# Kernel optimization log

Hardware: AMD Instinct MI355X
Metric: run time of the kernel (lower is better)

Reference implementation:

```python
import jax, jax.numpy as jnp
import numpy as np
import math

D_MODEL = 1024
N_HEADS = 16
SEQ = 1024
BATCH = 4


def setup_inputs() -> dict:
    key = jax.random.key(0)
    ks = jax.random.split(key, 13)
    s = 1.0 / math.sqrt(D_MODEL)  # keep logits in a sane range
    return {
        "x": jax.random.normal(ks[0], (BATCH, SEQ, D_MODEL), jnp.float32),
        "Wq": jax.random.normal(ks[1], (D_MODEL, D_MODEL), jnp.float32) * s,
        "bq": jnp.zeros((D_MODEL,), jnp.float32),
        "Wk": jax.random.normal(ks[2], (D_MODEL, D_MODEL), jnp.float32) * s,
        "bk": jnp.zeros((D_MODEL,), jnp.float32),
        "Wv": jax.random.normal(ks[3], (D_MODEL, D_MODEL), jnp.float32) * s,
        "bv": jnp.zeros((D_MODEL,), jnp.float32),
        "Wo": jax.random.normal(ks[4], (D_MODEL, D_MODEL), jnp.float32) * s,
        "bo": jnp.zeros((D_MODEL,), jnp.float32),
        "Wimp": jax.random.normal(ks[5], (N_HEADS, D_MODEL), jnp.float32) * s,
        "bimp": jnp.zeros((N_HEADS,), jnp.float32),
        "k_ema": jax.random.normal(ks[6], (SEQ, D_MODEL), jnp.float32),
        "v_ema": jax.random.normal(ks[7], (SEQ, D_MODEL), jnp.float32),
    }


def reference(x, Wq, bq, Wk, bk, Wv, bv, Wo, bo, Wimp, bimp, k_ema, v_ema):
    B, S, D = x.shape
    H = Wimp.shape[0]
    hd = D // H

    def proj(W, b):
        # [B,S,D] -> [B,H,S,hd]
        return (x @ W.T + b).reshape(B, S, H, hd).transpose(0, 2, 1, 3)

    q = proj(Wq, bq)
    k = proj(Wk, bk)
    v = proj(Wv, bv)

    scores = jnp.einsum("bhqd,bhkd->bhqk", q, k) / math.sqrt(hd)

    # importance bias: outer-sum of per-head key/value importance vectors
    k_imp = (k_ema[:S] @ Wimp.T + bimp).T  # [H, S]
    v_imp = (v_ema[:S] @ Wimp.T + bimp).T  # [H, S]
    bias = 0.5 * (k_imp[:, :, None] + v_imp[:, None, :])  # [H, S, S]
    scores = scores + 0.1 * bias[None]

    # causal mask (torch masks before bias add; -inf + finite == -inf, so equivalent)
    causal = jnp.triu(jnp.ones((S, S), bool), k=1)
    scores = jnp.where(causal, -jnp.inf, scores)

    attn = jax.nn.softmax(scores, axis=-1)
    out = jnp.einsum("bhqk,bhkd->bhqd", attn, v)
    out = out.transpose(0, 2, 1, 3).reshape(B, S, D)
    return out @ Wo.T + bo
```

## Files before the change

kernel.cpp:

```cpp
#include <hip/hip_runtime.h>
#include <hip/hip_bf16.h>
#include <math.h>

#define D_MODEL 1024
#define SEQ     1024
#define BATCH   4
#define NHEADS  16
#define HD      64

#define QSC 0.18033688f
#define BSC 0.072134752f

typedef __bf16 bf16x8 __attribute__((ext_vector_type(8)));
typedef __bf16 bf16x4 __attribute__((ext_vector_type(4)));
typedef float  f32x4  __attribute__((ext_vector_type(4)));

__device__ __forceinline__ f32x4 mfma16(bf16x8 a, bf16x8 b, f32x4 c) {
  return __builtin_amdgcn_mfma_f32_16x16x32_bf16(a, b, c, 0, 0, 0);
}

__device__ __forceinline__ void async16(__bf16* lds, const __bf16* g) {
  __builtin_amdgcn_global_load_lds(g, lds, 16, 0, 0);
}

__device__ __forceinline__ float fexp2(float x) {
  float r;
  asm volatile("v_exp_f32 %0, %1" : "=v"(r) : "v"(x));
  return r;
}

__global__ __launch_bounds__(256) void prep_kernel(
    const float* __restrict__ x,
    const float* __restrict__ Wq, const float* __restrict__ Wk,
    const float* __restrict__ Wv, const float* __restrict__ Wo,
    const float* __restrict__ v_ema,
    const float* __restrict__ Wimp, const float* __restrict__ bimp,
    __bf16* __restrict__ x_bf, __bf16* __restrict__ wq_bf, __bf16* __restrict__ wk_bf,
    __bf16* __restrict__ wv_bf, __bf16* __restrict__ wo_bf,
    float* __restrict__ vimp) {
  const int bid = blockIdx.x;
  const int tid = threadIdx.x;
  if (bid < 4096) {
    int i = bid * 256 + tid;
    float4 v = ((const float4*)x)[i];
    bf16x4 o; o[0] = (__bf16)v.x; o[1] = (__bf16)v.y; o[2] = (__bf16)v.z; o[3] = (__bf16)v.w;
    ((bf16x4*)x_bf)[i] = o;
  } else if (bid < 8192) {
    int i = (bid - 4096) * 256 + tid;
    int sel = i >> 18;
    int j = i & 262143;
    const float* s = (sel == 0) ? Wq : (sel == 1) ? Wk : (sel == 2) ? Wv : Wo;
    __bf16* d      = (sel == 0) ? wq_bf : (sel == 1) ? wk_bf : (sel == 2) ? wv_bf : wo_bf;
    float4 v = ((const float4*)s)[j];
    bf16x4 o; o[0] = (__bf16)v.x; o[1] = (__bf16)v.y; o[2] = (__bf16)v.z; o[3] = (__bf16)v.w;
    ((bf16x4*)d)[j] = o;
  } else {
    const int s    = (bid - 8192) * 4 + (tid >> 6);
    const int lane = tid & 63;
    const float4* ve = (const float4*)(v_ema + (size_t)s * D_MODEL);
    float acc0 = 0.f, acc1 = 0.f, acc2 = 0.f, acc3 = 0.f;
    float acc4 = 0.f, acc5 = 0.f, acc6 = 0.f, acc7 = 0.f;
    float acc8 = 0.f, acc9 = 0.f, accA = 0.f, accB = 0.f;
    float accC = 0.f, accD = 0.f, accE = 0.f, accF = 0.f;
    #pragma unroll
    for (int i = 0; i < 4; i++) {
      const int c = lane + i * 64;
      float4 v = ve[c];
      #define VIMP_H(H, ACC)                                                     \
        {                                                                        \
          float4 w = ((const float4*)(Wimp + (H) * D_MODEL))[c];                 \
          ACC += v.x * w.x + v.y * w.y + v.z * w.z + v.w * w.w;                  \
        }
      VIMP_H(0, acc0)  VIMP_H(1, acc1)  VIMP_H(2, acc2)  VIMP_H(3, acc3)
      VIMP_H(4, acc4)  VIMP_H(5, acc5)  VIMP_H(6, acc6)  VIMP_H(7, acc7)
      VIMP_H(8, acc8)  VIMP_H(9, acc9)  VIMP_H(10, accA) VIMP_H(11, accB)
      VIMP_H(12, accC) VIMP_H(13, accD) VIMP_H(14, accE) VIMP_H(15, accF)
      #undef VIMP_H
    }
    #define VIMP_RED(ACC)                                                        \
      for (int mm = 32; mm >= 1; mm >>= 1) ACC += __shfl_xor(ACC, mm);
    VIMP_RED(acc0) VIMP_RED(acc1) VIMP_RED(acc2) VIMP_RED(acc3)
    VIMP_RED(acc4) VIMP_RED(acc5) VIMP_RED(acc6) VIMP_RED(acc7)
    VIMP_RED(acc8) VIMP_RED(acc9) VIMP_RED(accA) VIMP_RED(accB)
    VIMP_RED(accC) VIMP_RED(accD) VIMP_RED(accE) VIMP_RED(accF)
    #undef VIMP_RED
    if (lane == 0) {
      vimp[0  * SEQ + s] = acc0 + bimp[0];  vimp[1  * SEQ + s] = acc1 + bimp[1];
      vimp[2  * SEQ + s] = acc2 + bimp[2];  vimp[3  * SEQ + s] = acc3 + bimp[3];
      vimp[4  * SEQ + s] = acc4 + bimp[4];  vimp[5  * SEQ + s] = acc5 + bimp[5];
      vimp[6  * SEQ + s] = acc6 + bimp[6];  vimp[7  * SEQ + s] = acc7 + bimp[7];
      vimp[8  * SEQ + s] = acc8 + bimp[8];  vimp[9  * SEQ + s] = acc9 + bimp[9];
      vimp[10 * SEQ + s] = accA + bimp[10]; vimp[11 * SEQ + s] = accB + bimp[11];
      vimp[12 * SEQ + s] = accC + bimp[12]; vimp[13 * SEQ + s] = accD + bimp[13];
      vimp[14 * SEQ + s] = accE + bimp[14]; vimp[15 * SEQ + s] = accF + bimp[15];
    }
  }
}

template<bool OUT_BF16>
__global__ __launch_bounds__(256) void gemm_bt(
    const __bf16* __restrict__ A,
    const __bf16* __restrict__ W0, const __bf16* __restrict__ W1, const __bf16* __restrict__ W2,
    const float* __restrict__ b0, const float* __restrict__ b1, const float* __restrict__ b2,
    void* out0, void* out1, void* out2, float sc0, float sc1, float sc2) {
  const int z = blockIdx.z;
  const __bf16* W   = (z == 0) ? W0 : (z == 1) ? W1 : W2;
  const float* bias = (z == 0) ? b0 : (z == 1) ? b1 : b2;
  void* out         = (z == 0) ? out0 : (z == 1) ? out1 : out2;
  const float sc    = (z == 0) ? sc0 : (z == 1) ? sc1 : sc2;

  __shared__ __bf16 As[4 * 4096];
  __shared__ __bf16 Bs[4 * 4096];

  const int tid = threadIdx.x;
  const int w = tid >> 6, l = tid & 63;
  const int quad = l >> 4, l16 = l & 15;
  const int wy = w >> 1, wx = w & 1;
  const int row0 = blockIdx.y * 128;
  const int col0 = blockIdx.x * 128;

  const f32x4 fzero = {0.f, 0.f, 0.f, 0.f};
  f32x4 acc[4][4];
  for (int i = 0; i < 4; i++)
    for (int j = 0; j < 4; j++) acc[i][j] = fzero;

  const int lr = l >> 2;
  const int sw0 = (((l & 3) ^ (lr & 3)) * 8);
  const int rowA = w * 16 + lr;
  const __bf16* aptr = A + (size_t)(row0 + rowA) * D_MODEL + sw0;
  const __bf16* bptr = W + (size_t)(col0 + rowA) * D_MODEL + sw0;
  const int ldsOff = w * 512 + l * 8;

  const int rswz = (quad ^ (l16 & 3)) * 8;

  #pragma unroll
  for (int p = 0; p < 3; ++p) {
    const int off = p << 12;
    const int kk = p * 32;
    async16(&As[off + ldsOff], aptr + kk);
    async16(&As[off + 2048 + ldsOff], aptr + (size_t)64 * D_MODEL + kk);
    async16(&Bs[off + ldsOff], bptr + kk);
    async16(&Bs[off + 2048 + ldsOff], bptr + (size_t)64 * D_MODEL + kk);
  }

  #pragma unroll 4
  for (int t = 0; t < 32; ++t) {
    const int rb = (t & 3) << 12;
    if (t < 29) {
      const int sb = ((t + 3) & 3) << 12;
      const int kk = (t + 3) * 32;
      async16(&As[sb + ldsOff], aptr + kk);
      async16(&As[sb + 2048 + ldsOff], aptr + (size_t)64 * D_MODEL + kk);
      async16(&Bs[sb + ldsOff], bptr + kk);
      async16(&Bs[sb + 2048 + ldsOff], bptr + (size_t)64 * D_MODEL + kk);
      asm volatile("s_waitcnt vmcnt(12)" ::: "memory");
    } else if (t == 29) {
      asm volatile("s_waitcnt vmcnt(8)" ::: "memory");
    } else if (t == 30) {
      asm volatile("s_waitcnt vmcnt(4)" ::: "memory");
    } else {
      asm volatile("s_waitcnt vmcnt(0)" ::: "memory");
    }
    __builtin_amdgcn_s_barrier();
    bf16x8 af[4], bfr[4];
    #pragma unroll
    for (int mi = 0; mi < 4; mi++) af[mi]  = *(const bf16x8*)&As[rb + (wy * 64 + mi * 16 + l16) * 32 + rswz];
    #pragma unroll
    for (int ni = 0; ni < 4; ni++) bfr[ni] = *(const bf16x8*)&Bs[rb + (wx * 64 + ni * 16 + l16) * 32 + rswz];
    if (z == 1) {
      #pragma unroll
      for (int mi = 0; mi < 4; mi++)
        #pragma unroll
        for (int ni = 0; ni < 4; ni++)
          acc[mi][ni] = mfma16(bfr[ni], af[mi], acc[mi][ni]);
    } else {
      #pragma unroll
      for (int mi = 0; mi < 4; mi++)
        #pragma unroll
        for (int ni = 0; ni < 4; ni++)
          acc[mi][ni] = mfma16(af[mi], bfr[ni], acc[mi][ni]);
    }
    __builtin_amdgcn_s_barrier();
  }

  if (z == 1 && OUT_BF16) {
    __bf16* kp = (__bf16*)out;
    #pragma unroll
    for (int ni = 0; ni < 4; ni++) {
      const int wcolbase = col0 + wx * 64 + ni * 16 + quad * 4;
      const float4 b4 = *(const float4*)&bias[wcolbase];
      const float bb[4] = {b4.x, b4.y, b4.z, b4.w};
      #pragma unroll
      for (int mi = 0; mi < 4; mi++) {
        const int token = row0 + wy * 64 + mi * 16 + l16;
        const int bh = (token >> 10) * 16 + (wcolbase >> 6);
        const int colp = ((wcolbase & 63) + ((token & 7) << 3)) & 63;
        union { __bf16 hh[4]; uint2 uu; } pk;
        #pragma unroll
        for (int r = 0; r < 4; r++) pk.hh[r] = (__bf16)(acc[mi][ni][r] + bb[r]);
        *(uint2*)(kp + ((size_t)bh * SEQ + (token & 1023)) * HD + colp) = pk.uu;
      }
    }
  } else if (z == 2 && OUT_BF16) {
    __bf16* vp = (__bf16*)out;
    #pragma unroll
    for (int ni = 0; ni < 4; ni++) {
      const int col = col0 + wx * 64 + ni * 16 + l16;
      const float bv = bias[col];
      #pragma unroll
      for (int mi = 0; mi < 4; mi++) {
        const int token = row0 + wy * 64 + mi * 16 + quad * 4;
        const int bh = (token >> 10) * 16 + (col >> 6);
        const int chk = (token >> 6) & 15;
        const int keyp = ((token & 63) + ((col & 7) << 3)) & 63;
        const size_t base = (((size_t)bh * 16 + chk) * 64 + (col & 63)) * 64 + keyp;
        union { __bf16 hh[4]; uint2 uu; } pk;
        #pragma unroll
        for (int r = 0; r < 4; r++) pk.hh[r] = (__bf16)(acc[mi][ni][r] + bv);
        *(uint2*)(vp + base) = pk.uu;
      }
    }
  } else {
    #pragma unroll
    for (int ni = 0; ni < 4; ni++) {
      const int col = col0 + wx * 64 + ni * 16 + l16;
      const float bv = bias[col];
      #pragma unroll
      for (int mi = 0; mi < 4; mi++) {
        const int row = row0 + wy * 64 + mi * 16 + quad * 4;
        #pragma unroll
        for (int r = 0; r < 4; r++) {
          float v = (acc[mi][ni][r] + bv) * sc;
          if (OUT_BF16) ((__bf16*)out)[(size_t)(row + r) * D_MODEL + col] = (__bf16)v;
          else          ((float*)out)[(size_t)(row + r) * D_MODEL + col] = v;
        }
      }
    }
  }
}

__global__ __launch_bounds__(256, 2) void attn_kernel(
    const __bf16* __restrict__ Qb, const __bf16* __restrict__ Kp,
    const __bf16* __restrict__ Vp, const float* __restrict__ vimp,
    __bf16* __restrict__ Ob) {
  const int id = blockIdx.x;
  const int bh = id & 63;
  const int gg = id >> 6;
  const int b = bh >> 4, h = bh & 15;
  const int tid = threadIdx.x;
  const int wave = tid >> 6, lane = tid & 63;
  const int quad = lane >> 4, l16 = lane & 15;

  __shared__ __bf16 Kl[3][4096];
  __shared__ __bf16 Vl[3][4096];
  __shared__ __bf16 Ps[4][16][72];

  const __bf16* kbase = Kp + (size_t)bh * (SEQ * HD);
  const __bf16* vbase = Vp + (size_t)bh * (SEQ * HD);
  const float* vimpH = vimp + h * SEQ;

  const int rot0 = ((quad + (l16 & 7)) & 7) * 8;
  const int rot1 = ((quad + 4 + (l16 & 7)) & 7) * 8;
  const int frow = l16 * 64;

  const int g0 = gg, g1 = 15 - gg;

  const int qrow0 = g0 * 64 + wave * 16 + l16;
  const int qrow1 = g1 * 64 + wave * 16 + l16;
  const __bf16* qp0 = Qb + (size_t)(b * SEQ + qrow0) * D_MODEL + h * HD;
  const __bf16* qp1 = Qb + (size_t)(b * SEQ + qrow1) * D_MODEL + h * HD;
  bf16x8 qA0 = *(const bf16x8*)(qp0 + quad * 8);
  bf16x8 qA1 = *(const bf16x8*)(qp0 + 32 + quad * 8);
  bf16x8 qB0 = *(const bf16x8*)(qp1 + quad * 8);
  bf16x8 qB1 = *(const bf16x8*)(qp1 + 32 + quad * 8);

  async16(&Kl[0][tid * 8], kbase + tid * 8);
  async16(&Kl[0][2048 + tid * 8], kbase + 2048 + tid * 8);
  async16(&Vl[0][tid * 8], vbase + tid * 8);
  async16(&Vl[0][2048 + tid * 8], vbase + 2048 + tid * 8);
  async16(&Kl[1][tid * 8], kbase + 4096 + tid * 8);
  async16(&Kl[1][2048 + 4096 / 2 * 0 + tid * 8 + 0], kbase + 4096 + 2048 + tid * 8);
  async16(&Vl[1][tid * 8], vbase + 4096 + tid * 8);
  async16(&Vl[1][2048 + tid * 8], vbase + 4096 + 2048 + tid * 8);

  float l0 = 0.f, l1 = 0.f;
  f32x4 o0[4], o1[4];
  #pragma unroll
  for (int td = 0; td < 4; td++) {
    o0[td][0] = 0.f; o0[td][1] = 0.f; o0[td][2] = 0.f; o0[td][3] = 0.f;
    o1[td][0] = 0.f; o1[td][1] = 0.f; o1[td][2] = 0.f; o1[td][3] = 0.f;
  }

  #pragma unroll 1
  for (int c = 0; c <= g1; ++c) {
    const int buf = c % 3;
    if (c < g1) asm volatile("s_waitcnt vmcnt(4)" ::: "memory");
    else        asm volatile("s_waitcnt vmcnt(0)" ::: "memory");
    __builtin_amdgcn_s_barrier();
    const int kc = c * 64;
    float4 vi[4];
    #pragma unroll
    for (int t = 0; t < 4; t++) vi[t] = *(const float4*)(vimpH + kc + t * 16 + quad * 4);
    __builtin_amdgcn_sched_barrier(0);
    if (c + 2 <= g1) {
      const int nb = (c + 2) % 3;
      const __bf16* gk = kbase + (size_t)(c + 2) * 4096;
      const __bf16* gv = vbase + (size_t)(c + 2) * 4096;
      async16(&Kl[nb][tid * 8], gk + tid * 8);
      async16(&Kl[nb][2048 + tid * 8], gk + 2048 + tid * 8);
      async16(&Vl[nb][tid * 8], gv + tid * 8);
      async16(&Vl[nb][2048 + tid * 8], gv + 2048 + tid * 8);
    }
    __builtin_amdgcn_sched_barrier(0);

    bf16x8 kf0[4], kf1[4], vfr0[4], vfr1[4];
    #pragma unroll
    for (int t = 0; t < 4; t++) {
      kf0[t] = *(const bf16x8*)&Kl[buf][t * 1024 + frow + rot0];
      kf1[t] = *(const bf16x8*)&Kl[buf][t * 1024 + frow + rot1];
    }
    #pragma unroll
    for (int td = 0; td < 4; td++) {
      vfr0[td] = *(const bf16x8*)&Vl[buf][td * 1024 + frow + rot0];
      vfr1[td] = *(const bf16x8*)&Vl[buf][td * 1024 + frow + rot1];
    }
    const f32x4 fz = {0.f, 0.f, 0.f, 0.f};

    {
      float p[4][4];
      float lsum = 0.f;
      #pragma unroll
      for (int t = 0; t < 4; t++) {
        f32x4 sacc = fz;
        sacc = mfma16(kf0[t], qB0, sacc);
        sacc = mfma16(kf1[t], qB1, sacc);
        const float vib[4] = {vi[t].x, vi[t].y, vi[t].z, vi[t].w};
        if (c == g1) {
          #pragma unroll
          for (int r = 0; r < 4; r++) {
            float pp = fexp2(sacc[r] + BSC * vib[r]);
            pp = (kc + t * 16 + quad * 4 + r <= qrow1) ? pp : 0.f;
            p[t][r] = pp;
            lsum += pp;
          }
        } else {
          #pragma unroll
          for (int r = 0; r < 4; r++) {
            float pp = fexp2(sacc[r] + BSC * vib[r]);
            p[t][r] = pp;
            lsum += pp;
          }
        }
      }
      l1 += lsum;
      #pragma unroll
      for (int t = 0; t < 4; t++) {
        union { __bf16 hh[4]; uint2 uu; } pk;
        #pragma unroll
        for (int r = 0; r < 4; r++) pk.hh[r] = (__bf16)p[t][r];
        *(uint2*)&Ps[wave][l16][t * 16 + quad * 4] = pk.uu;
      }
      bf16x8 pf0 = *(const bf16x8*)&Ps[wave][l16][quad * 8];
      bf16x8 pf1 = *(const bf16x8*)&Ps[wave][l16][32 + quad * 8];
      #pragma unroll
      for (int td = 0; td < 4; td++) {
        o1[td] = mfma16(vfr0[td], pf0, o1[td]);
        o1[td] = mfma16(vfr1[td], pf1, o1[td]);
      }
    }

    if (c <= g0) {
      float p[4][4];
      float lsum = 0.f;
      #pragma unroll
      for (int t = 0; t < 4; t++) {
        f32x4 sacc = fz;
        sacc = mfma16(kf0[t], qA0, sacc);
        sacc = mfma16(kf1[t], qA1, sacc);
        const float vib[4] = {vi[t].x, vi[t].y, vi[t].z, vi[t].w};
        if (c == g0) {
          #pragma unroll
          for (int r = 0; r < 4; r++) {
            float pp = fexp2(sacc[r] + BSC * vib[r]);
            pp = (kc + t * 16 + quad * 4 + r <= qrow0) ? pp : 0.f;
            p[t][r] = pp;
            lsum += pp;
          }
        } else {
          #pragma unroll
          for (int r = 0; r < 4; r++) {
            float pp = fexp2(sacc[r] + BSC * vib[r]);
            p[t][r] = pp;
            lsum += pp;
          }
        }
      }
      l0 += lsum;
      #pragma unroll
      for (int t = 0; t < 4; t++) {
        union { __bf16 hh[4]; uint2 uu; } pk;
        #pragma unroll
        for (int r = 0; r < 4; r++) pk.hh[r] = (__bf16)p[t][r];
        *(uint2*)&Ps[wave][l16][t * 16 + quad * 4] = pk.uu;
      }
      bf16x8 pf0 = *(const bf16x8*)&Ps[wave][l16][quad * 8];
      bf16x8 pf1 = *(const bf16x8*)&Ps[wave][l16][32 + quad * 8];
      #pragma unroll
      for (int td = 0; td < 4; td++) {
        o0[td] = mfma16(vfr0[td], pf0, o0[td]);
        o0[td] = mfma16(vfr1[td], pf1, o0[td]);
      }
      if (c == g0) {
        float L = l0;
        L += __shfl_xor(L, 16);
        L += __shfl_xor(L, 32);
        const float il = 1.0f / L;
        __bf16* op = Ob + (size_t)(b * SEQ + qrow0) * D_MODEL + h * HD;
        #pragma unroll
        for (int td = 0; td < 4; td++) {
          union { __bf16 hh[4]; uint2 uu; } pk;
          #pragma unroll
          for (int r = 0; r < 4; r++) pk.hh[r] = (__bf16)(o0[td][r] * il);
          *(uint2*)(op + td * 16 + quad * 4) = pk.uu;
        }
      }
    }
  }

  float L = l1;
  L += __shfl_xor(L, 16);
  L += __shfl_xor(L, 32);
  const float il = 1.0f / L;
  __bf16* op = Ob + (size_t)(b * SEQ + qrow1) * D_MODEL + h * HD;
  #pragma unroll
  for (int td = 0; td < 4; td++) {
    union { __bf16 hh[4]; uint2 uu; } pk;
    #pragma unroll
    for (int r = 0; r < 4; r++) pk.hh[r] = (__bf16)(o1[td][r] * il);
    *(uint2*)(op + td * 16 + quad * 4) = pk.uu;
  }
}

extern "C" void kernel_launch(void* const* d_in, const int* in_sizes, int n_in,
                              void* d_out, int out_size, void* d_ws, size_t ws_size,
                              hipStream_t stream) {
  const float* x     = (const float*)d_in[0];
  const float* Wq    = (const float*)d_in[1];
  const float* bq    = (const float*)d_in[2];
  const float* Wk    = (const float*)d_in[3];
  const float* bk    = (const float*)d_in[4];
  const float* Wv    = (const float*)d_in[5];
  const float* bv    = (const float*)d_in[6];
  const float* Wo    = (const float*)d_in[7];
  const float* bo    = (const float*)d_in[8];
  const float* Wimp  = (const float*)d_in[9];
  const float* bimp  = (const float*)d_in[10];
  const float* v_ema = (const float*)d_in[12];
  float* out = (float*)d_out;

  char* ws = (char*)d_ws;
  __bf16* x_bf  = (__bf16*)(ws);
  __bf16* wq_bf = (__bf16*)(ws + (8ull  << 20));
  __bf16* wk_bf = (__bf16*)(ws + (10ull << 20));
  __bf16* wv_bf = (__bf16*)(ws + (12ull << 20));
  __bf16* wo_bf = (__bf16*)(ws + (14ull << 20));
  __bf16* q_bf  = (__bf16*)(ws + (16ull << 20));
  __bf16* kp_bf = (__bf16*)(ws + (24ull << 20));
  __bf16* vp_bf = (__bf16*)(ws + (32ull << 20));
  __bf16* a_bf  = (__bf16*)(ws + (40ull << 20));
  float*  vimp  = (float*)(ws + (48ull << 20));

  prep_kernel<<<8448, 256, 0, stream>>>(
      x, Wq, Wk, Wv, Wo, v_ema, Wimp, bimp,
      x_bf, wq_bf, wk_bf, wv_bf, wo_bf, vimp);

  gemm_bt<true><<<dim3(8, 32, 3), 256, 0, stream>>>(
      x_bf, wq_bf, wk_bf, wv_bf, bq, bk, bv,
      (void*)q_bf, (void*)kp_bf, (void*)vp_bf, QSC, 1.0f, 1.0f);

  attn_kernel<<<dim3(512), 256, 0, stream>>>(
      q_bf, kp_bf, vp_bf, vimp, a_bf);

  gemm_bt<false><<<dim3(8, 32, 1), 256, 0, stream>>>(
      a_bf, wo_bf, wo_bf, wo_bf, bo, bo, bo,
      (void*)out, (void*)out, (void*)out, 1.0f, 1.0f, 1.0f);
}
```

Baseline: 206.4 us.

## Switch projection GEMM to BK=64 double-buffered pipeline with 8-way swizzle

Restructures the bf16 GEMM mainloop from a 4-stage ring of K=32 tiles into a 2-stage double buffer of K=64 tiles. The loop count halves to 16 and each iteration runs two MFMA k-steps between barriers. The XOR swizzle widens to 8 chunks to match the 64-element LDS row. This cuts barrier and waitcnt overhead per FLOP but gives less prefetch depth, which may expose more global-load latency.

```diff
diff --git a/kernel.cpp b/kernel.cpp
--- a/kernel.cpp
+++ b/kernel.cpp
@@ -109,8 +109,8 @@
   void* out         = (z == 0) ? out0 : (z == 1) ? out1 : out2;
   const float sc    = (z == 0) ? sc0 : (z == 1) ? sc1 : sc2;
 
-  __shared__ __bf16 As[4 * 4096];
-  __shared__ __bf16 Bs[4 * 4096];
+  __shared__ __bf16 As[2 * 8192];
+  __shared__ __bf16 Bs[2 * 8192];
 
   const int tid = threadIdx.x;
   const int w = tid >> 6, l = tid & 63;
@@ -124,61 +124,58 @@
   for (int i = 0; i < 4; i++)
     for (int j = 0; j < 4; j++) acc[i][j] = fzero;
 
-  const int lr = l >> 2;
-  const int sw0 = (((l & 3) ^ (lr & 3)) * 8);
-  const int rowA = w * 16 + lr;
-  const __bf16* aptr = A + (size_t)(row0 + rowA) * D_MODEL + sw0;
-  const __bf16* bptr = W + (size_t)(col0 + rowA) * D_MODEL + sw0;
-  const int ldsOff = w * 512 + l * 8;
-
-  const int rswz = (quad ^ (l16 & 3)) * 8;
+  const int rk = tid >> 3;
+  const int csw = (((tid & 7) ^ (rk & 7)) * 8);
+  const int tid8 = tid * 8;
+  const __bf16* aS = A + (size_t)(row0 + rk) * D_MODEL + csw;
+  const __bf16* bS = W + (size_t)(col0 + rk) * D_MODEL + csw;
+
+  const int pch0 = ((0 * 4 + quad) ^ (l16 & 7)) * 8;
+  const int pch1 = ((1 * 4 + quad) ^ (l16 & 7)) * 8;
 
   #pragma unroll
-  for (int p = 0; p < 3; ++p) {
-    const int off = p << 12;
-    const int kk = p * 32;
-    async16(&As[off + ldsOff], aptr + kk);
-    async16(&As[off + 2048 + ldsOff], aptr + (size_t)64 * D_MODEL + kk);
-    async16(&Bs[off + ldsOff], bptr + kk);
-    async16(&Bs[off + 2048 + ldsOff], bptr + (size_t)64 * D_MODEL + kk);
-  }
-
-  #pragma unroll 4
-  for (int t = 0; t < 32; ++t) {
-    const int rb = (t & 3) << 12;
-    if (t < 29) {
-      const int sb = ((t + 3) & 3) << 12;
-      const int kk = (t + 3) * 32;
-      async16(&As[sb + ldsOff], aptr + kk);
-      async16(&As[sb + 2048 + ldsOff], aptr + (size_t)64 * D_MODEL + kk);
-      async16(&Bs[sb + ldsOff], bptr + kk);
-      async16(&Bs[sb + 2048 + ldsOff], bptr + (size_t)64 * D_MODEL + kk);
-      asm volatile("s_waitcnt vmcnt(12)" ::: "memory");
-    } else if (t == 29) {
+  for (int p = 0; p < 4; ++p) {
+    async16(&As[p * 2048 + tid8], aS + (size_t)p * 32 * D_MODEL);
+    async16(&Bs[p * 2048 + tid8], bS + (size_t)p * 32 * D_MODEL);
+  }
+
+  #pragma unroll 2
+  for (int t = 0; t < 16; ++t) {
+    const int rb = (t & 1) << 13;
+    if (t < 15) {
+      const int sb = ((t + 1) & 1) << 13;
+      const size_t kk = (size_t)(t + 1) * 64;
+      #pragma unroll
+      for (int p = 0; p < 4; ++p) {
+        async16(&As[sb + p * 2048 + tid8], aS + (size_t)p * 32 * D_MODEL + kk);
+        async16(&Bs[sb + p * 2048 + tid8], bS + (size_t)p * 32 * D_MODEL + kk);
+      }
       asm volatile("s_waitcnt vmcnt(8)" ::: "memory");
-    } else if (t == 30) {
-      asm volatile("s_waitcnt vmcnt(4)" ::: "memory");
     } else {
       asm volatile("s_waitcnt vmcnt(0)" ::: "memory");
     }
     __builtin_amdgcn_s_barrier();
-    bf16x8 af[4], bfr[4];
-    #pragma unroll
-    for (int mi = 0; mi < 4; mi++) af[mi]  = *(const bf16x8*)&As[rb + (wy * 64 + mi * 16 + l16) * 32 + rswz];
-    #pragma unroll
-    for (int ni = 0; ni < 4; ni++) bfr[ni] = *(const bf16x8*)&Bs[rb + (wx * 64 + ni * 16 + l16) * 32 + rswz];
-    if (z == 1) {
-      #pragma unroll
-      for (int mi = 0; mi < 4; mi++)
-        #pragma unroll
-        for (int ni = 0; ni < 4; ni++)
-          acc[mi][ni] = mfma16(bfr[ni], af[mi], acc[mi][ni]);
-    } else {
-      #pragma unroll
-      for (int mi = 0; mi < 4; mi++)
-        #pragma unroll
-        for (int ni = 0; ni < 4; ni++)
-          acc[mi][ni] = mfma16(af[mi], bfr[ni], acc[mi][ni]);
+    #pragma unroll
+    for (int ks = 0; ks < 2; ++ks) {
+      const int pch = ks ? pch1 : pch0;
+      bf16x8 af[4], bfr[4];
+      #pragma unroll
+      for (int mi = 0; mi < 4; mi++) af[mi]  = *(const bf16x8*)&As[rb + (wy * 64 + mi * 16 + l16) * 64 + pch];
+      #pragma unroll
+      for (int ni = 0; ni < 4; ni++) bfr[ni] = *(const bf16x8*)&Bs[rb + (wx * 64 + ni * 16 + l16) * 64 + pch];
+      if (z == 1) {
+        #pragma unroll
+        for (int mi = 0; mi < 4; mi++)
+          #pragma unroll
+          for (int ni = 0; ni < 4; ni++)
+            acc[mi][ni] = mfma16(bfr[ni], af[mi], acc[mi][ni]);
+      } else {
+        #pragma unroll
+        for (int mi = 0; mi < 4; mi++)
+          #pragma unroll
+          for (int ni = 0; ni < 4; ni++)
+            acc[mi][ni] = mfma16(af[mi], bfr[ni], acc[mi][ni]);
+      }
     }
     __builtin_amdgcn_s_barrier();
   }
@@ -279,7 +276,7 @@
   async16(&Vl[0][tid * 8], vbase + tid * 8);
   async16(&Vl[0][2048 + tid * 8], vbase + 2048 + tid * 8);
   async16(&Kl[1][tid * 8], kbase + 4096 + tid * 8);
-  async16(&Kl[1][2048 + 4096 / 2 * 0 + tid * 8 + 0], kbase + 4096 + 2048 + tid * 8);
+  async16(&Kl[1][2048 + tid * 8], kbase + 4096 + 2048 + tid * 8);
   async16(&Vl[1][tid * 8], vbase + 4096 + tid * 8);
   async16(&Vl[1][2048 + tid * 8], vbase + 4096 + 2048 + tid * 8);
 
```

Result: faster. 198.2 us (-4.0%).
